# Performance work log

Hardware: AMD Instinct MI355X
Metric: run time of the kernel (lower is better)

The kernel has to match this reference:

```python
import jax, jax.numpy as jnp
import numpy as np

B, N, C = 8, 2048, 256
E = 32768
H, C_OUT = 8, 64
NEG_SLOPE = 0.2


def setup_inputs() -> dict:
    key = jax.random.key(0)
    k1, k2, k3, k4, k5 = jax.random.split(key, 5)
    x = jax.random.normal(k1, (B, N, C), dtype=jnp.float32)
    edge_index = jax.random.randint(k2, (2, E), 0, N, dtype=jnp.int64)
    W_lin = jax.random.normal(k3, (C, H * C_OUT), dtype=jnp.float32) * 0.05
    att_src = jax.random.normal(k4, (H, C_OUT), dtype=jnp.float32) * 0.05
    att_dst = jax.random.normal(k5, (H, C_OUT), dtype=jnp.float32) * 0.05
    bias = jnp.zeros((H * C_OUT,), dtype=jnp.float32)
    return {"x": x, "edge_index": edge_index, "W_lin": W_lin,
            "att_src": att_src, "att_dst": att_dst, "bias": bias}


def _segment_softmax(logits, segment_ids, num_segments):
    # stable softmax over edges grouped by destination node
    seg_max = jax.ops.segment_max(logits, segment_ids, num_segments=num_segments)
    logits = logits - seg_max[segment_ids]
    exp = jnp.exp(logits)
    seg_sum = jax.ops.segment_sum(exp, segment_ids, num_segments=num_segments)
    return exp / (seg_sum[segment_ids] + 1e-16)


def reference(x, edge_index, W_lin, att_src, att_dst, bias):
    Bn = B * N
    # node linear projection -> [B*N, H, C_out]
    xt = (x.reshape(Bn, C) @ W_lin).reshape(Bn, H, C_OUT)

    # batch the shared edge_index: block b offset by b*N, then append self-loops
    offs = (jnp.arange(B, dtype=edge_index.dtype) * N)[None, :, None]  # [1,B,1]
    ei = (edge_index[:, None, :] + offs).reshape(2, B * E)              # [2,B*E]
    loops = jnp.arange(Bn, dtype=edge_index.dtype)
    src = jnp.concatenate([ei[0], loops])
    dst = jnp.concatenate([ei[1], loops])

    x_j = xt[src]  # [E_tot, H, C_out] source features
    x_i = xt[dst]
    alpha = jnp.einsum('ehc,hc->eh', x_j, att_src) + jnp.einsum('ehc,hc->eh', x_i, att_dst)
    alpha = jax.nn.leaky_relu(alpha, NEG_SLOPE)
    alpha = _segment_softmax(alpha, dst, Bn)  # softmax over incoming edges per node/head

    msg = x_j * alpha[:, :, None]
    out = jax.ops.segment_sum(msg, dst, num_segments=Bn)  # [B*N, H, C_out]
    out = out.reshape(B, N, H * C_OUT) + bias
    return out
```

## Files before the change

### kernel.cpp

```cpp
#include <hip/hip_runtime.h>
#include <hip/hip_bf16.h>

#define BDIM 8
#define NNODE 2048
#define CIN 256
#define NEDGE 32768
#define NHEAD 8
#define COUT 64
#define HC 512
#define BN_TOT 16384
#define NEG_SLOPE 0.2f
#define GEMM_BLKS 256
#define CAP 64

typedef __hip_bfloat16 bf16;
typedef __attribute__((ext_vector_type(8))) short bfrag;
typedef __attribute__((ext_vector_type(4))) float ffrag;
typedef float f32x2 __attribute__((ext_vector_type(2)));
typedef float fv4 __attribute__((ext_vector_type(4)));

static __device__ __forceinline__ short f2b(float f) {
    __hip_bfloat16 h = __float2bfloat16(f);
    return *(short*)&h;
}
static __device__ __forceinline__ unsigned pack2(float a, float b) {
    return (unsigned)(unsigned short)f2b(a) | ((unsigned)(unsigned short)f2b(b) << 16);
}
static __device__ __forceinline__ void pkfma(f32x2& a, f32x2 x, f32x2 w) {
    asm("v_pk_fma_f32 %0, %1, %2, %0" : "+v"(a) : "v"(x), "v"(w));
}
static __device__ __forceinline__ f32x2 unpack2(unsigned v) {
    f32x2 r;
    r.x = __uint_as_float(v << 16);
    r.y = __uint_as_float(v & 0xffff0000u);
    return r;
}
static __device__ __forceinline__ void async_cp16(const short* gsrc, short* ldst) {
    __builtin_amdgcn_global_load_lds(
        (const __attribute__((address_space(1))) void*)gsrc,
        (__attribute__((address_space(3))) void*)ldst, 16, 0, 0);
}

__global__ __launch_bounds__(256) void prep_kernel(const float* __restrict__ W,
                                                   short* __restrict__ WT,
                                                   int* __restrict__ cnt) {
    const int b = blockIdx.x;
    if (b < 128) {
        __shared__ float t[32][33];
        const int kt = b >> 4;
        const int nt = b & 15;
        const int tx = threadIdx.x & 31, ty = threadIdx.x >> 5;
#pragma unroll
        for (int i = 0; i < 4; ++i)
            t[ty + 8 * i][tx] = W[(kt * 32 + ty + 8 * i) * HC + nt * 32 + tx];
        __syncthreads();
#pragma unroll
        for (int i = 0; i < 4; ++i)
            WT[(nt * 32 + ty + 8 * i) * CIN + kt * 32 + tx] = f2b(t[tx][ty + 8 * i]);
    } else {
        for (int k = threadIdx.x; k < NNODE; k += 256) cnt[k] = 0;
    }
}

__global__ __launch_bounds__(512, 2) void gemm_scatter(const float* __restrict__ x,
                                                       const short* __restrict__ WT,
                                                       short* __restrict__ xtb,
                                                       const float* __restrict__ att_src,
                                                       const float* __restrict__ att_dst,
                                                       float* __restrict__ ssrc,
                                                       float* __restrict__ sdst,
                                                       const int* __restrict__ ei,
                                                       int* __restrict__ cnt,
                                                       int* __restrict__ col) {
    __shared__ __align__(16) short As[64 * 256];
    __shared__ __align__(16) short Bs[2][512 * 32];

    const int gblk = blockIdx.x;
    const int tid  = threadIdx.x;

    if (gblk < 64) {
        const int t = gblk * 512 + tid;
        const int s = ei[t];
        const int d = ei[NEDGE + t];
        const int p = atomicAdd(&cnt[d], 1);
        if (p < CAP) col[d * CAP + p] = s;
    }

    const int tile = (gblk & 7) * 32 + (gblk >> 3);
    const int lane = tid & 63;
    const int w    = tid >> 6;
    const int row0 = tile * 64;
    const int fm   = lane & 15;
    const int fq   = lane >> 4;

    {
        const int r   = tid >> 3;
        const int kb0 = (tid & 7) * 8;
#pragma unroll
        for (int i = 0; i < 4; ++i) {
            const int kb = kb0 + i * 64;
            fv4 v0 = __builtin_nontemporal_load((const fv4*)&x[(row0 + r) * CIN + kb]);
            fv4 v1 = __builtin_nontemporal_load((const fv4*)&x[(row0 + r) * CIN + kb + 4]);
            bfrag o;
            o[0] = f2b(v0.x); o[1] = f2b(v0.y); o[2] = f2b(v0.z); o[3] = f2b(v0.w);
            o[4] = f2b(v1.x); o[5] = f2b(v1.y); o[6] = f2b(v1.z); o[7] = f2b(v1.w);
            *(bfrag*)&As[(((r >> 4) * 32 + (kb >> 3)) * 16 + (r & 15)) * 8] = o;
        }
    }

    {
#pragma unroll
        for (int i2 = 0; i2 < 4; ++i2) {
            const int cb16 = w * 4 + i2;
            const int c = cb16 * 16 + (lane >> 2);
            async_cp16(&WT[c * CIN + (lane & 3) * 8], &Bs[0][cb16 * 512]);
        }
    }
    __syncthreads();

    ffrag acc[4][4] = {};

#pragma unroll
    for (int k8 = 0; k8 < 8; ++k8) {
        const int buf = k8 & 1;
        if (k8 < 7) {
            asm volatile("s_waitcnt lgkmcnt(0)" ::: "memory");
            __builtin_amdgcn_sched_barrier(0);
            const int k0n = (k8 + 1) * 32;
#pragma unroll
            for (int i2 = 0; i2 < 4; ++i2) {
                const int cb16 = w * 4 + i2;
                const int c = cb16 * 16 + (lane >> 2);
                async_cp16(&WT[c * CIN + k0n + (lane & 3) * 8], &Bs[buf ^ 1][cb16 * 512]);
            }
            asm volatile("s_waitcnt vmcnt(4)" ::: "memory");
        } else {
            asm volatile("s_waitcnt vmcnt(0)" ::: "memory");
        }
        __builtin_amdgcn_sched_barrier(0);

        bfrag af[4], bfv[4];
#pragma unroll
        for (int mg = 0; mg < 4; ++mg)
            af[mg] = *(const bfrag*)&As[((mg * 32 + k8 * 4 + fq) * 16 + fm) * 8];
#pragma unroll
        for (int ng = 0; ng < 4; ++ng)
            bfv[ng] = *(const bfrag*)&Bs[buf][(((w * 4 + ng) * 16 + fm) * 4 + fq) * 8];
#pragma unroll
        for (int ng = 0; ng < 4; ++ng)
#pragma unroll
            for (int mg = 0; mg < 4; ++mg)
                acc[mg][ng] = __builtin_amdgcn_mfma_f32_16x16x32_bf16(
                    bfv[ng], af[mg], acc[mg][ng], 0, 0, 0);
    }

    float4 s4[4], d4[4];
#pragma unroll
    for (int ng = 0; ng < 4; ++ng) {
        const int cb = w * 64 + ng * 16 + fq * 4;
        s4[ng] = *(const float4*)&att_src[cb];
        d4[ng] = *(const float4*)&att_dst[cb];
    }
#pragma unroll
    for (int mg = 0; mg < 4; ++mg) {
        const int nd = row0 + mg * 16 + fm;
        float ps = 0.f, pd = 0.f;
#pragma unroll
        for (int ng = 0; ng < 4; ++ng) {
            const int cb = w * 64 + ng * 16 + fq * 4;
            uint2 pk;
            pk.x = pack2(acc[mg][ng][0], acc[mg][ng][1]);
            pk.y = pack2(acc[mg][ng][2], acc[mg][ng][3]);
            *(uint2*)&xtb[nd * HC + cb] = pk;
            ps += acc[mg][ng][0] * s4[ng].x + acc[mg][ng][1] * s4[ng].y +
                  acc[mg][ng][2] * s4[ng].z + acc[mg][ng][3] * s4[ng].w;
            pd += acc[mg][ng][0] * d4[ng].x + acc[mg][ng][1] * d4[ng].y +
                  acc[mg][ng][2] * d4[ng].z + acc[mg][ng][3] * d4[ng].w;
        }
        ps += __shfl_xor(ps, 16); ps += __shfl_xor(ps, 32);
        pd += __shfl_xor(pd, 16); pd += __shfl_xor(pd, 32);
        if (lane < 16) {
            ssrc[nd * NHEAD + w] = ps;
            sdst[nd * NHEAD + w] = pd;
        }
    }
}

__global__ __launch_bounds__(256) void aggregate(const short* __restrict__ xtb,
                                                 const float* __restrict__ ssrc,
                                                 const float* __restrict__ sdst,
                                                 const int* __restrict__ cnt,
                                                 const int* __restrict__ col,
                                                 const float* __restrict__ bias,
                                                 float* __restrict__ out) {
    __shared__ float wlds[4][NHEAD][68];
    __shared__ int   jlds[4][64];
    const int nb   = threadIdx.x >> 6;
    const int lane = threadIdx.x & 63;
    const int blk  = blockIdx.x;
    const int bidx = blk & 7;
    const int boff = bidx * NNODE;
    const int i    = boff + (blk >> 3) * 4 + nb;
    const int n    = i & (NNODE - 1);
    const int deg  = min(cnt[n], CAP);
    const int start = n * CAP;
    const int h    = lane >> 3;
    const int sub  = lane & 7;
    float* wrow = &wlds[nb][0][0];
    int*   jrow = &jlds[nb][0];

    for (int t = lane; t < NHEAD * 68; t += 64) wrow[t] = 0.f;
    jrow[lane] = i;

    const float sdh = sdst[i * NHEAD + h];
    float selfv = ssrc[i * NHEAD + h] + sdh;
    selfv = selfv >= 0.f ? selfv : NEG_SLOPE * selfv;
    const float eself = __expf(selfv);

    float sp = 0.f;
    for (int e = sub; e < deg; e += 8) {
        int j = boff + col[start + e];
        float v = ssrc[j * NHEAD + h] + sdh;
        v = v >= 0.f ? v : NEG_SLOPE * v;
        float wv = __expf(v);
        wrow[h * 68 + e] = wv;
        if (h == 0) jrow[e] = j;
        sp += wv;
    }
    sp += __shfl_xor(sp, 4); sp += __shfl_xor(sp, 2); sp += __shfl_xor(sp, 1);
    const float inv = 1.f / (sp + eself + 1e-16f);

    const int c8 = lane * 8;
    f32x2 acc2[4] = {};

    {
        uint4 xv = *(const uint4*)&xtb[i * HC + c8];
        f32x2 ev = {eself, eself};
        pkfma(acc2[0], unpack2(xv.x), ev);
        pkfma(acc2[1], unpack2(xv.y), ev);
        pkfma(acc2[2], unpack2(xv.z), ev);
        pkfma(acc2[3], unpack2(xv.w), ev);
    }

    const int degp = (deg + 7) & ~7;
    for (int e0 = 0; e0 < degp; e0 += 8) {
        float4 wA = *(const float4*)&wrow[h * 68 + e0];
        float4 wB = *(const float4*)&wrow[h * 68 + e0 + 4];
        int4 jA = *(const int4*)&jrow[e0];
        int4 jB = *(const int4*)&jrow[e0 + 4];
        uint4 x0 = *(const uint4*)&xtb[jA.x * HC + c8];
        uint4 x1 = *(const uint4*)&xtb[jA.y * HC + c8];
        uint4 x2 = *(const uint4*)&xtb[jA.z * HC + c8];
        uint4 x3 = *(const uint4*)&xtb[jA.w * HC + c8];
        uint4 x4 = *(const uint4*)&xtb[jB.x * HC + c8];
        uint4 x5 = *(const uint4*)&xtb[jB.y * HC + c8];
        uint4 x6 = *(const uint4*)&xtb[jB.z * HC + c8];
        uint4 x7 = *(const uint4*)&xtb[jB.w * HC + c8];
        f32x2 w0 = {wA.x, wA.x}, w1 = {wA.y, wA.y}, w2 = {wA.z, wA.z}, w3 = {wA.w, wA.w};
        f32x2 w4 = {wB.x, wB.x}, w5 = {wB.y, wB.y}, w6 = {wB.z, wB.z}, w7 = {wB.w, wB.w};
#define ACC_EDGE(xv, wv)                       \
        pkfma(acc2[0], unpack2(xv.x), wv);     \
        pkfma(acc2[1], unpack2(xv.y), wv);     \
        pkfma(acc2[2], unpack2(xv.z), wv);     \
        pkfma(acc2[3], unpack2(xv.w), wv);
        ACC_EDGE(x0, w0) ACC_EDGE(x1, w1) ACC_EDGE(x2, w2) ACC_EDGE(x3, w3)
        ACC_EDGE(x4, w4) ACC_EDGE(x5, w5) ACC_EDGE(x6, w6) ACC_EDGE(x7, w7)
#undef ACC_EDGE
    }

    const float4 b0 = *(const float4*)&bias[c8];
    const float4 b1 = *(const float4*)&bias[c8 + 4];
    fv4 o0 = {acc2[0].x * inv + b0.x, acc2[0].y * inv + b0.y,
              acc2[1].x * inv + b0.z, acc2[1].y * inv + b0.w};
    fv4 o1 = {acc2[2].x * inv + b1.x, acc2[2].y * inv + b1.y,
              acc2[3].x * inv + b1.z, acc2[3].y * inv + b1.w};
    __builtin_nontemporal_store(o0, (fv4*)&out[i * HC + c8]);
    __builtin_nontemporal_store(o1, (fv4*)&out[i * HC + c8 + 4]);
}

extern "C" void kernel_launch(void* const* d_in, const int* in_sizes, int n_in,
                              void* d_out, int out_size, void* d_ws, size_t ws_size,
                              hipStream_t stream) {
    const float* x       = (const float*)d_in[0];
    const int*   ei      = (const int*)d_in[1];
    const float* W       = (const float*)d_in[2];
    const float* att_src = (const float*)d_in[3];
    const float* att_dst = (const float*)d_in[4];
    const float* bias    = (const float*)d_in[5];
    float* out = (float*)d_out;

    char* ws = (char*)d_ws;
    short* xtb  = (short*)(ws);
    float* ssrc = (float*)(ws + 16777216);
    float* sdst = (float*)(ws + 17301504);
    int*   cnt  = (int*)(ws + 17825792);
    int*   col  = (int*)(ws + 17833984);
    short* WT   = (short*)(ws + 18358272);
    prep_kernel<<<129, 256, 0, stream>>>(W, WT, cnt);
    gemm_scatter<<<GEMM_BLKS, 512, 0, stream>>>(x, WT, xtb, att_src, att_dst,
                                                ssrc, sdst, ei, cnt, col);
    aggregate<<<BN_TOT / 4, 256, 0, stream>>>(xtb, ssrc, sdst, cnt, col, bias, out);
}
```

Before: 122.4 us.

## Replace LDS staging of edge weights and indices with wave shuffles

The aggregate kernel no longer stages per-edge softmax weights and source indices in shared memory. Each group of 8 edges is now processed as it is produced: each lane computes one weight, and the weights and indices are broadcast with __shfl before the gather-FMA, all in one fused loop. This drops the LDS zero-fill and the LDS reads and writes, but it adds two shuffles per edge and puts the exp computation on the gather loop's critical path, so load latency may be exposed more.

```diff
diff --git a/kernel.cpp b/kernel.cpp
--- a/kernel.cpp
+++ b/kernel.cpp
@@ -193,10 +193,8 @@
                                                  const int* __restrict__ col,
                                                  const float* __restrict__ bias,
                                                  float* __restrict__ out) {
-    __shared__ float wlds[4][NHEAD][68];
-    __shared__ int   jlds[4][64];
+    const int lane = threadIdx.x & 63;
     const int nb   = threadIdx.x >> 6;
-    const int lane = threadIdx.x & 63;
     const int blk  = blockIdx.x;
     const int bidx = blk & 7;
     const int boff = bidx * NNODE;
@@ -206,31 +204,13 @@
     const int start = n * CAP;
     const int h    = lane >> 3;
     const int sub  = lane & 7;
-    float* wrow = &wlds[nb][0][0];
-    int*   jrow = &jlds[nb][0];
-
-    for (int t = lane; t < NHEAD * 68; t += 64) wrow[t] = 0.f;
-    jrow[lane] = i;
+    const int c8   = lane * 8;
 
     const float sdh = sdst[i * NHEAD + h];
     float selfv = ssrc[i * NHEAD + h] + sdh;
     selfv = selfv >= 0.f ? selfv : NEG_SLOPE * selfv;
     const float eself = __expf(selfv);
 
-    float sp = 0.f;
-    for (int e = sub; e < deg; e += 8) {
-        int j = boff + col[start + e];
-        float v = ssrc[j * NHEAD + h] + sdh;
-        v = v >= 0.f ? v : NEG_SLOPE * v;
-        float wv = __expf(v);
-        wrow[h * 68 + e] = wv;
-        if (h == 0) jrow[e] = j;
-        sp += wv;
-    }
-    sp += __shfl_xor(sp, 4); sp += __shfl_xor(sp, 2); sp += __shfl_xor(sp, 1);
-    const float inv = 1.f / (sp + eself + 1e-16f);
-
-    const int c8 = lane * 8;
     f32x2 acc2[4] = {};
 
     {
@@ -242,31 +222,31 @@
         pkfma(acc2[3], unpack2(xv.w), ev);
     }
 
-    const int degp = (deg + 7) & ~7;
-    for (int e0 = 0; e0 < degp; e0 += 8) {
-        float4 wA = *(const float4*)&wrow[h * 68 + e0];
-        float4 wB = *(const float4*)&wrow[h * 68 + e0 + 4];
-        int4 jA = *(const int4*)&jrow[e0];
-        int4 jB = *(const int4*)&jrow[e0 + 4];
-        uint4 x0 = *(const uint4*)&xtb[jA.x * HC + c8];
-        uint4 x1 = *(const uint4*)&xtb[jA.y * HC + c8];
-        uint4 x2 = *(const uint4*)&xtb[jA.z * HC + c8];
-        uint4 x3 = *(const uint4*)&xtb[jA.w * HC + c8];
-        uint4 x4 = *(const uint4*)&xtb[jB.x * HC + c8];
-        uint4 x5 = *(const uint4*)&xtb[jB.y * HC + c8];
-        uint4 x6 = *(const uint4*)&xtb[jB.z * HC + c8];
-        uint4 x7 = *(const uint4*)&xtb[jB.w * HC + c8];
-        f32x2 w0 = {wA.x, wA.x}, w1 = {wA.y, wA.y}, w2 = {wA.z, wA.z}, w3 = {wA.w, wA.w};
-        f32x2 w4 = {wB.x, wB.x}, w5 = {wB.y, wB.y}, w6 = {wB.z, wB.z}, w7 = {wB.w, wB.w};
-#define ACC_EDGE(xv, wv)                       \
-        pkfma(acc2[0], unpack2(xv.x), wv);     \
-        pkfma(acc2[1], unpack2(xv.y), wv);     \
-        pkfma(acc2[2], unpack2(xv.z), wv);     \
-        pkfma(acc2[3], unpack2(xv.w), wv);
-        ACC_EDGE(x0, w0) ACC_EDGE(x1, w1) ACC_EDGE(x2, w2) ACC_EDGE(x3, w3)
-        ACC_EDGE(x4, w4) ACC_EDGE(x5, w5) ACC_EDGE(x6, w6) ACC_EDGE(x7, w7)
-#undef ACC_EDGE
-    }
+    float sp = 0.f;
+    for (int e0 = 0; e0 < deg; e0 += 8) {
+        int jme = i;
+        float wv = 0.f;
+        if (e0 + sub < deg) {
+            jme = boff + col[start + e0 + sub];
+            float v = ssrc[jme * NHEAD + h] + sdh;
+            v = v >= 0.f ? v : NEG_SLOPE * v;
+            wv = __expf(v);
+        }
+        sp += wv;
+#pragma unroll
+        for (int k = 0; k < 8; ++k) {
+            const int   jk = __shfl(jme, k);
+            const float wk = __shfl(wv, (h << 3) | k);
+            uint4 xr = *(const uint4*)&xtb[jk * HC + c8];
+            f32x2 wk2 = {wk, wk};
+            pkfma(acc2[0], unpack2(xr.x), wk2);
+            pkfma(acc2[1], unpack2(xr.y), wk2);
+            pkfma(acc2[2], unpack2(xr.z), wk2);
+            pkfma(acc2[3], unpack2(xr.w), wk2);
+        }
+    }
+    sp += __shfl_xor(sp, 4); sp += __shfl_xor(sp, 2); sp += __shfl_xor(sp, 1);
+    const float inv = 1.f / (sp + eself + 1e-16f);
 
     const float4 b0 = *(const float4*)&bias[c8];
     const float4 b1 = *(const float4*)&bias[c8 + 4];
```

Measured after the change: 120.2 us (median of 2 runs). No clear change (-1.8%).
